# Kernel optimization log

Hardware: AMD Instinct MI355X
Metric: run time of the kernel (lower is better)

## Reference

```python
import jax, jax.numpy as jnp
import numpy as np

SCAD_A = 3.7
PERCENTILE_Q = 0.75
EPS = 1e-8
LAM_HAT = 0.9
PROP_STEP = 4


def setup_inputs() -> dict:
    key = jax.random.key(0)
    ks = jax.random.split(key, 4)
    N, IN, H, OUT = 4096, 512, 256, 64
    p = 32.0 / N  # avg degree ~32 (pre-symmetrization ~64 after OR, still sparse)
    u = jax.random.uniform(ks[0], (N, N))
    Au = u < p
    Asym = Au | Au.T
    eye = jnp.eye(N, dtype=bool)
    A = jnp.where(eye, 0.0, Asym.astype(jnp.float32))  # zero diagonal; add_loops adds I
    X = jax.random.normal(ks[1], (N, IN), dtype=jnp.float32)
    W1 = jax.random.normal(ks[2], (IN, H), dtype=jnp.float32) / np.sqrt(IN)
    b1 = jnp.zeros((H,), dtype=jnp.float32)
    W2 = jax.random.normal(ks[3], (H, OUT), dtype=jnp.float32) / np.sqrt(H)
    b2 = jnp.zeros((OUT,), dtype=jnp.float32)
    log_gamma_0 = jnp.asarray(np.log(3.0), dtype=jnp.float32)
    raw_decay = jnp.asarray(np.log(0.85 / 0.15), dtype=jnp.float32)
    raw_alpha_blend = jnp.asarray(0.0, dtype=jnp.float32)  # sigmoid -> 0.5 blend
    return {"A": A, "X": X, "W1": W1, "b1": b1, "W2": W2, "b2": b2,
            "log_gamma_0": log_gamma_0, "raw_decay": raw_decay,
            "raw_alpha_blend": raw_alpha_blend}


def _scad_weight(y, lam, a):
    # SCAD-derived reweighting: 1 for y<=lam, (a*lam - y)/((a-1)*y) in the middle, 0 beyond a*lam.
    y_safe = jnp.maximum(y, EPS)  # avoid inf/nan in unselected branch (forward value unchanged)
    w_mid = (a * lam - y) / ((a - 1.0) * y_safe)
    return jnp.where(y <= lam, 1.0, jnp.where(y <= a * lam, w_mid, 0.0))


def reference(A, X, W1, b1, W2, b2, log_gamma_0, raw_decay, raw_alpha_blend):
    N = A.shape[0]
    eye = jnp.eye(N, dtype=A.dtype)
    Ahat = A + eye                          # add_loops
    D = Ahat.sum(-1)                        # [N]
    D_sq = jnp.sqrt(D)[:, None]             # [N,1]
    A_tilde = Ahat / (D_sq * D_sq.T)        # sym_norm: D^{-1/2} A D^{-1/2}
    edge_mask = (Ahat > 0) & (eye == 0)     # A_bool & ~I
    has_edges = edge_mask.sum() > 0

    # MLP (eval mode: dropout inactive)
    F0 = jnp.maximum(X @ W1 + b1, 0.0) @ W2 + b2   # [N, out_dim]

    alpha = jax.nn.sigmoid(raw_alpha_blend)
    g0 = jnp.exp(log_gamma_0)
    r = jax.nn.sigmoid(raw_decay)
    lam = 1.0 / LAM_HAT - 1.0

    Fc = F0
    for k in range(PROP_STEP):
        gamma_param_k = g0 * (r ** k)
        Fn = Fc / D_sq
        nrm = jnp.linalg.norm(Fn, axis=-1, keepdims=True)
        Fu = Fn / jnp.maximum(nrm, EPS)     # F.normalize semantics
        y = jnp.clip(1.0 - Fu @ Fu.T, 0.0, 2.0)  # [N,N] cosine distance
        y = jax.lax.stop_gradient(y)        # y.detach()
        y_edges = jnp.where(edge_mask, y, jnp.nan)
        gamma_data_k = jnp.nanquantile(y_edges, PERCENTILE_Q)
        gamma_data_k = jnp.maximum(jnp.where(has_edges, gamma_data_k, 1.0), EPS)
        lam_combined = alpha * (gamma_param_k / SCAD_A) + (1.0 - alpha) * (gamma_data_k / SCAD_A)
        W = _scad_weight(y, lam_combined, SCAD_A)
        W = W * (1.0 - eye)
        W = jnp.where(jnp.isnan(W), 1.0, W)
        Q_hat = ((W * Ahat).sum(-1) / D + lam)[:, None]
        Fc = (W * A_tilde) @ Fc / Q_hat + lam * F0 / Q_hat
    return Fc
```

## Files before the change

### kernel.cpp

```cpp
#include <hip/hip_runtime.h>
#include <math.h>

#define N_NODES 4096
#define IN_DIM  512
#define H_DIM   256
#define OUT_DIM 64
#define SCAD_Af 3.7f
#define EPSf    1e-8f
#define NBINS   8192
#define MAXE    524288
#define MAXD    256
#define KSPLIT  4

__global__ void k_degfill(const float* __restrict__ A, int* __restrict__ tmpcols,
                          int* __restrict__ rowcnt, float* __restrict__ D,
                          float* __restrict__ isD) {
    int i = blockIdx.x;
    __shared__ int cnt;
    if (threadIdx.x == 0) cnt = 0;
    __syncthreads();
    const float* row = A + (size_t)i * N_NODES;
    for (int j = threadIdx.x; j < N_NODES; j += blockDim.x) {
        if (row[j] != 0.0f) {
            int p = atomicAdd(&cnt, 1);
            if (p < MAXD) tmpcols[i * MAXD + p] = j;
        }
    }
    __syncthreads();
    if (threadIdx.x == 0) {
        int t = cnt;
        rowcnt[i] = t;
        float d = (float)t + 1.0f;
        D[i] = d;
        isD[i] = 1.0f / sqrtf(d);
    }
}

__global__ void k_scan(const int* __restrict__ rowcnt, int* __restrict__ rowptr) {
    __shared__ int sh[1024];
    int t = threadIdx.x;
    int v0 = rowcnt[4 * t + 0], v1 = rowcnt[4 * t + 1];
    int v2 = rowcnt[4 * t + 2], v3 = rowcnt[4 * t + 3];
    int s = v0 + v1 + v2 + v3;
    sh[t] = s;
    __syncthreads();
    for (int off = 1; off < 1024; off <<= 1) {
        int x = 0;
        if (t >= off) x = sh[t - off];
        __syncthreads();
        sh[t] += x;
        __syncthreads();
    }
    int excl = sh[t] - s;
    rowptr[4 * t + 0] = excl;
    rowptr[4 * t + 1] = excl + v0;
    rowptr[4 * t + 2] = excl + v0 + v1;
    rowptr[4 * t + 3] = excl + v0 + v1 + v2;
    if (t == 1023) rowptr[N_NODES] = sh[1023];
}

__global__ void k_compact(const int* __restrict__ tmpcols, const int* __restrict__ rowcnt,
                          const int* __restrict__ rowptr, int* __restrict__ colIdx) {
    int i = blockIdx.x;
    int n = rowcnt[i], base = rowptr[i];
    for (int p = threadIdx.x; p < n; p += blockDim.x)
        colIdx[base + p] = tmpcols[i * MAXD + p];
}

__global__ void k_gemm1_part(const float* __restrict__ X, const float* __restrict__ W1,
                             float* __restrict__ part) {
    const int K = IN_DIM, Nn = H_DIM;
    __shared__ float As[16][68];
    __shared__ float Bs[16][64];
    int tx = threadIdx.x & 15, ty = threadIdx.x >> 4;
    int bm = blockIdx.y * 64, bn = blockIdx.x * 64;
    int kbeg = blockIdx.z * (K / KSPLIT), kend = kbeg + K / KSPLIT;
    float acc[4][4] = {};
    for (int k0 = kbeg; k0 < kend; k0 += 16) {
        {
            int r = threadIdx.x >> 2, kv = threadIdx.x & 3;
            float4 v = *(const float4*)(X + (size_t)(bm + r) * K + k0 + kv * 4);
            As[kv * 4 + 0][r] = v.x;
            As[kv * 4 + 1][r] = v.y;
            As[kv * 4 + 2][r] = v.z;
            As[kv * 4 + 3][r] = v.w;
        }
        {
            int kk = threadIdx.x >> 4, nv = threadIdx.x & 15;
            *(float4*)&Bs[kk][nv * 4] =
                *(const float4*)(W1 + (size_t)(k0 + kk) * Nn + bn + nv * 4);
        }
        __syncthreads();
#pragma unroll
        for (int kk = 0; kk < 16; kk++) {
            float a[4], b[4];
#pragma unroll
            for (int u = 0; u < 4; u++) { a[u] = As[kk][ty * 4 + u]; b[u] = Bs[kk][tx * 4 + u]; }
#pragma unroll
            for (int u = 0; u < 4; u++)
#pragma unroll
                for (int v = 0; v < 4; v++) acc[u][v] += a[u] * b[v];
        }
        __syncthreads();
    }
    float* Cm = part + (size_t)blockIdx.z * N_NODES * H_DIM;
#pragma unroll
    for (int u = 0; u < 4; u++) {
        int m = bm + ty * 4 + u;
#pragma unroll
        for (int v = 0; v < 4; v++)
            Cm[(size_t)m * Nn + bn + tx * 4 + v] = acc[u][v];
    }
}

__global__ void k_fuse1(const float* __restrict__ part, const float* __restrict__ bias,
                        float* __restrict__ H1) {
    int idx = blockIdx.x * blockDim.x + threadIdx.x;
    const size_t tot = (size_t)N_NODES * H_DIM / 4;
    const float4* p = (const float4*)part;
    float4 a = p[idx], b = p[tot + idx], c = p[2 * tot + idx], d = p[3 * tot + idx];
    float4 bb = ((const float4*)bias)[idx & (H_DIM / 4 - 1)];
    float4 r;
    r.x = fmaxf(a.x + b.x + c.x + d.x + bb.x, 0.0f);
    r.y = fmaxf(a.y + b.y + c.y + d.y + bb.y, 0.0f);
    r.z = fmaxf(a.z + b.z + c.z + d.z + bb.z, 0.0f);
    r.w = fmaxf(a.w + b.w + c.w + d.w + bb.w, 0.0f);
    ((float4*)H1)[idx] = r;
}

__global__ void k_gemm2(const float* __restrict__ Am, const float* __restrict__ Bm,
                        const float* __restrict__ bias, float* __restrict__ Cm) {
    const int Nn = OUT_DIM, K = H_DIM;
    __shared__ float As[16][68];
    __shared__ float Bs[16][64];
    int tx = threadIdx.x & 15, ty = threadIdx.x >> 4;
    int bm = blockIdx.y * 64, bn = 0;
    float acc[4][4] = {};
    for (int k0 = 0; k0 < K; k0 += 16) {
        {
            int r = threadIdx.x >> 2, kv = threadIdx.x & 3;
            float4 v = *(const float4*)(Am + (size_t)(bm + r) * K + k0 + kv * 4);
            As[kv * 4 + 0][r] = v.x;
            As[kv * 4 + 1][r] = v.y;
            As[kv * 4 + 2][r] = v.z;
            As[kv * 4 + 3][r] = v.w;
        }
        {
            int kk = threadIdx.x >> 4, nv = threadIdx.x & 15;
            *(float4*)&Bs[kk][nv * 4] =
                *(const float4*)(Bm + (size_t)(k0 + kk) * Nn + bn + nv * 4);
        }
        __syncthreads();
#pragma unroll
        for (int kk = 0; kk < 16; kk++) {
            float a[4], b[4];
#pragma unroll
            for (int u = 0; u < 4; u++) { a[u] = As[kk][ty * 4 + u]; b[u] = Bs[kk][tx * 4 + u]; }
#pragma unroll
            for (int u = 0; u < 4; u++)
#pragma unroll
                for (int v = 0; v < 4; v++) acc[u][v] += a[u] * b[v];
        }
        __syncthreads();
    }
#pragma unroll
    for (int u = 0; u < 4; u++) {
        int m = bm + ty * 4 + u;
#pragma unroll
        for (int v = 0; v < 4; v++) {
            int n = bn + tx * 4 + v;
            Cm[(size_t)m * Nn + n] = acc[u][v] + bias[n];
        }
    }
}

__global__ void k_norm(const float* __restrict__ Fc, const float* __restrict__ isD,
                       float* __restrict__ Fu, unsigned int* __restrict__ hist) {
    int gid = blockIdx.x * blockDim.x + threadIdx.x;
    if (gid < NBINS) hist[gid] = 0u;
    int i = gid >> 6, c = gid & 63;
    float fn = Fc[(size_t)i * 64 + c] * isD[i];
    float s = fn * fn;
    for (int off = 32; off; off >>= 1) s += __shfl_xor(s, off, 64);
    float nrm = sqrtf(s);
    Fu[(size_t)i * 64 + c] = fn / fmaxf(nrm, EPSf);
}

__global__ void k_edgehist(const float* __restrict__ Fu, const int* __restrict__ rowptr,
                           const int* __restrict__ colIdx, float* __restrict__ y_e,
                           unsigned int* __restrict__ hist) {
    __shared__ unsigned int hl[NBINS];
    for (int b = threadIdx.x; b < NBINS; b += blockDim.x) hl[b] = 0u;
    __syncthreads();
    int gid = blockIdx.x * blockDim.x + threadIdx.x;
    int i = gid >> 6;
    int lane = threadIdx.x & 63;
    int g = lane >> 2, l = lane & 3;
    int e0 = rowptr[i], e1 = rowptr[i + 1];
    const float4* Fu4 = (const float4*)Fu;
    float4 fi0 = Fu4[i * 16 + l * 4 + 0];
    float4 fi1 = Fu4[i * 16 + l * 4 + 1];
    float4 fi2 = Fu4[i * 16 + l * 4 + 2];
    float4 fi3 = Fu4[i * 16 + l * 4 + 3];
    for (int base = e0; base < e1; base += 16) {
        int e = base + g;
        bool act = e < e1;
        int j = act ? colIdx[e] : i;
        float4 a0 = Fu4[(size_t)j * 16 + l * 4 + 0];
        float4 a1 = Fu4[(size_t)j * 16 + l * 4 + 1];
        float4 a2 = Fu4[(size_t)j * 16 + l * 4 + 2];
        float4 a3 = Fu4[(size_t)j * 16 + l * 4 + 3];
        float s = fi0.x * a0.x + fi0.y * a0.y + fi0.z * a0.z + fi0.w * a0.w
                + fi1.x * a1.x + fi1.y * a1.y + fi1.z * a1.z + fi1.w * a1.w
                + fi2.x * a2.x + fi2.y * a2.y + fi2.z * a2.z + fi2.w * a2.w
                + fi3.x * a3.x + fi3.y * a3.y + fi3.z * a3.z + fi3.w * a3.w;
        s += __shfl_xor(s, 1, 64);
        s += __shfl_xor(s, 2, 64);
        if (act && l == 0) {
            float y = 1.0f - s;
            y = fminf(fmaxf(y, 0.0f), 2.0f);
            y_e[e] = y;
            int bin = (int)(y * (NBINS * 0.5f));
            if (bin > NBINS - 1) bin = NBINS - 1;
            atomicAdd(&hl[bin], 1u);
        }
    }
    __syncthreads();
    for (int b = threadIdx.x; b < NBINS; b += blockDim.x) {
        unsigned int v = hl[b];
        if (v) atomicAdd(&hist[b], v);
    }
}

__device__ __forceinline__ float scad_w(float y, float lamc) {
    if (y <= lamc) return 1.0f;
    if (y <= SCAD_Af * lamc)
        return (SCAD_Af * lamc - y) / ((SCAD_Af - 1.0f) * fmaxf(y, EPSf));
    return 0.0f;
}

__global__ void k_propq(const unsigned int* __restrict__ hist,
                        const int* __restrict__ rowptr, const int* __restrict__ colIdx,
                        const float* __restrict__ y_e, const float* __restrict__ Fc,
                        const float* __restrict__ F0, const float* __restrict__ D,
                        const float* __restrict__ isD,
                        const float* __restrict__ lg0, const float* __restrict__ rdec,
                        const float* __restrict__ ralpha, int kiter,
                        float* __restrict__ Fout) {
    __shared__ unsigned int psum[256];
    __shared__ float vv[2];
    __shared__ float sh_scal;
    int t = threadIdx.x;
    {
        unsigned int cnt[32];
        const uint4* h4 = (const uint4*)hist;
        unsigned int s = 0;
#pragma unroll
        for (int q = 0; q < 8; q++) {
            uint4 v = h4[t * 8 + q];
            cnt[q * 4 + 0] = v.x; cnt[q * 4 + 1] = v.y;
            cnt[q * 4 + 2] = v.z; cnt[q * 4 + 3] = v.w;
            s += v.x + v.y + v.z + v.w;
        }
        psum[t] = s;
        __syncthreads();
        for (int off = 1; off < 256; off <<= 1) {
            unsigned int x = 0;
            if (t >= off) x = psum[t - off];
            __syncthreads();
            psum[t] += x;
            __syncthreads();
        }
        int nE = rowptr[N_NODES];
        double h = 0.75 * (double)(nE - 1);
        long long i0 = (long long)h;
        float frac = (float)(h - (double)i0);
        unsigned int r0 = (unsigned int)i0, r1 = (unsigned int)(i0 + 1);
        unsigned int cum = (t == 0) ? 0u : psum[t - 1];
#pragma unroll
        for (int b = 0; b < 32; b++) {
            unsigned int cn = cnt[b];
            unsigned int lo = cum;
            cum += cn;
            if (cn) {
                float v = ((float)(t * 32 + b) + 0.5f) * (2.0f / (float)NBINS);
                if (lo <= r0 && r0 < cum) vv[0] = v;
                if (lo <= r1 && r1 < cum) vv[1] = v;
            }
        }
        __syncthreads();
        if (t == 0) {
            float gd = vv[0] + frac * (vv[1] - vv[0]);
            gd = fmaxf(gd, EPSf);
            float alpha = 1.0f / (1.0f + expf(-ralpha[0]));
            float g0 = expf(lg0[0]);
            float r = 1.0f / (1.0f + expf(-rdec[0]));
            float gp = g0;
            for (int q = 0; q < kiter; q++) gp *= r;
            sh_scal = alpha * (gp / SCAD_Af) + (1.0f - alpha) * (gd / SCAD_Af);
        }
        __syncthreads();
    }
    float lamc = sh_scal;
    const float lam = (float)(1.0 / 0.9 - 1.0);
    int gid = blockIdx.x * blockDim.x + t;
    int i = gid >> 6, c = gid & 63;
    int e0 = rowptr[i], e1 = rowptr[i + 1];
    float acc = 0.0f, wsum = 0.0f;
    for (int base = e0; base < e1; base += 64) {
        int m = e1 - base; if (m > 64) m = 64;
        int   jl = (c < m) ? colIdx[base + c] : 0;
        float yl = (c < m) ? y_e[base + c] : 9.0f;
        float il = (c < m) ? isD[jl] : 0.0f;
        int tt = 0;
        for (; tt + 4 <= m; tt += 4) {
            int j0 = __shfl(jl, tt, 64),     j1 = __shfl(jl, tt + 1, 64);
            int j2 = __shfl(jl, tt + 2, 64), j3 = __shfl(jl, tt + 3, 64);
            float f0 = Fc[(size_t)j0 * 64 + c], f1 = Fc[(size_t)j1 * 64 + c];
            float f2 = Fc[(size_t)j2 * 64 + c], f3 = Fc[(size_t)j3 * 64 + c];
            float s0 = scad_w(__shfl(yl, tt, 64),     lamc);
            float s1 = scad_w(__shfl(yl, tt + 1, 64), lamc);
            float s2 = scad_w(__shfl(yl, tt + 2, 64), lamc);
            float s3 = scad_w(__shfl(yl, tt + 3, 64), lamc);
            wsum += s0 + s1 + s2 + s3;
            acc += s0 * __shfl(il, tt, 64) * f0 + s1 * __shfl(il, tt + 1, 64) * f1
                 + s2 * __shfl(il, tt + 2, 64) * f2 + s3 * __shfl(il, tt + 3, 64) * f3;
        }
        for (; tt < m; tt++) {
            int   j = __shfl(jl, tt, 64);
            float y = __shfl(yl, tt, 64);
            float w = scad_w(y, lamc);
            wsum += w;
            acc += w * __shfl(il, tt, 64) * Fc[(size_t)j * 64 + c];
        }
    }
    float Q = wsum / D[i] + lam;
    Fout[(size_t)i * 64 + c] = (isD[i] * acc + lam * F0[(size_t)i * 64 + c]) / Q;
}

extern "C" void kernel_launch(void* const* d_in, const int* in_sizes, int n_in,
                              void* d_out, int out_size, void* d_ws, size_t ws_size,
                              hipStream_t stream) {
    const float* A      = (const float*)d_in[0];
    const float* X      = (const float*)d_in[1];
    const float* W1     = (const float*)d_in[2];
    const float* b1     = (const float*)d_in[3];
    const float* W2     = (const float*)d_in[4];
    const float* b2     = (const float*)d_in[5];
    const float* lg0    = (const float*)d_in[6];
    const float* rdec   = (const float*)d_in[7];
    const float* ralpha = (const float*)d_in[8];
    float* out = (float*)d_out;

    char* w = (char*)d_ws;
    size_t off = 0;
    auto carve = [&](size_t bytes) -> char* {
        char* p = w + off;
        off += (bytes + 255) & ~(size_t)255;
        return p;
    };
    int*      rowcnt = (int*)carve(N_NODES * 4);
    int*      rowptr = (int*)carve((N_NODES + 16) * 4);
    int*      colIdx = (int*)carve(MAXE * 4);
    float*    y_e    = (float*)carve(MAXE * 4);
    unsigned* hist   = (unsigned*)carve(NBINS * 4);
    float*    D      = (float*)carve(N_NODES * 4);
    float*    isD    = (float*)carve(N_NODES * 4);
    float*    Fu     = (float*)carve((size_t)N_NODES * 64 * 4);
    float*    H1     = (float*)carve((size_t)N_NODES * H_DIM * 4);
    float*    part   = (float*)carve((size_t)KSPLIT * N_NODES * H_DIM * 4);
    float*    F0     = (float*)carve((size_t)N_NODES * 64 * 4);
    float*    FcA    = (float*)carve((size_t)N_NODES * 64 * 4);
    float*    FcB    = (float*)carve((size_t)N_NODES * 64 * 4);
    int*      tmpcols = (int*)part;

    k_degfill<<<dim3(N_NODES), dim3(256), 0, stream>>>(A, tmpcols, rowcnt, D, isD);
    k_scan<<<dim3(1), dim3(1024), 0, stream>>>(rowcnt, rowptr);
    k_compact<<<dim3(N_NODES), dim3(64), 0, stream>>>(tmpcols, rowcnt, rowptr, colIdx);

    k_gemm1_part<<<dim3(H_DIM / 64, N_NODES / 64, KSPLIT), dim3(256), 0, stream>>>(X, W1, part);
    k_fuse1<<<dim3(N_NODES * H_DIM / 4 / 256), dim3(256), 0, stream>>>(part, b1, H1);
    k_gemm2<<<dim3(1, N_NODES / 64), dim3(256), 0, stream>>>(H1, W2, b2, F0);

    const float* fin = F0;
    float* fouts[4] = {FcA, FcB, FcA, out};
    for (int k = 0; k < 4; k++) {
        k_norm<<<dim3(1024), dim3(256), 0, stream>>>(fin, isD, Fu, hist);
        k_edgehist<<<dim3(1024), dim3(256), 0, stream>>>(Fu, rowptr, colIdx, y_e, hist);
        k_propq<<<dim3(1024), dim3(256), 0, stream>>>(hist, rowptr, colIdx, y_e, fin, F0,
                                                      D, isD, lg0, rdec, ralpha, k, fouts[k]);
        fin = fouts[k];
    }
}
```

Before: 384.3 us.

## Fuse setup kernels, use padded CSR, fold normalization into propagation

Merges the degree scan and GEMM1 into one launch that splits work by block index. It also replaces the prefix-scan/compaction CSR with a fixed-stride padded adjacency (MAXD per row), fuses bias+ReLU+GEMM2 and the first normalization into one kernel, and moves per-iteration normalization into the propagation kernel with double-buffered histograms. This cuts the launch count from 18 to 10 and removes intermediate buffers such as H1. The cost is that GEMM2 now runs as a naive per-thread dot product that re-reads the four partial sums from global memory for every output column. It also drops the MAXD overflow guard on colIdx writes.

```diff
diff --git a/kernel.cpp b/kernel.cpp
--- a/kernel.cpp
+++ b/kernel.cpp
@@ -8,288 +8,241 @@
 #define SCAD_Af 3.7f
 #define EPSf    1e-8f
 #define NBINS   8192
-#define MAXE    524288
 #define MAXD    256
 #define KSPLIT  4
 
-__global__ void k_degfill(const float* __restrict__ A, int* __restrict__ tmpcols,
-                          int* __restrict__ rowcnt, float* __restrict__ D,
-                          float* __restrict__ isD) {
-    int i = blockIdx.x;
-    __shared__ int cnt;
-    if (threadIdx.x == 0) cnt = 0;
-    __syncthreads();
-    const float* row = A + (size_t)i * N_NODES;
-    for (int j = threadIdx.x; j < N_NODES; j += blockDim.x) {
-        if (row[j] != 0.0f) {
-            int p = atomicAdd(&cnt, 1);
-            if (p < MAXD) tmpcols[i * MAXD + p] = j;
-        }
-    }
-    __syncthreads();
-    if (threadIdx.x == 0) {
-        int t = cnt;
-        rowcnt[i] = t;
-        float d = (float)t + 1.0f;
-        D[i] = d;
-        isD[i] = 1.0f / sqrtf(d);
-    }
-}
-
-__global__ void k_scan(const int* __restrict__ rowcnt, int* __restrict__ rowptr) {
-    __shared__ int sh[1024];
-    int t = threadIdx.x;
-    int v0 = rowcnt[4 * t + 0], v1 = rowcnt[4 * t + 1];
-    int v2 = rowcnt[4 * t + 2], v3 = rowcnt[4 * t + 3];
-    int s = v0 + v1 + v2 + v3;
-    sh[t] = s;
-    __syncthreads();
-    for (int off = 1; off < 1024; off <<= 1) {
-        int x = 0;
-        if (t >= off) x = sh[t - off];
-        __syncthreads();
-        sh[t] += x;
-        __syncthreads();
-    }
-    int excl = sh[t] - s;
-    rowptr[4 * t + 0] = excl;
-    rowptr[4 * t + 1] = excl + v0;
-    rowptr[4 * t + 2] = excl + v0 + v1;
-    rowptr[4 * t + 3] = excl + v0 + v1 + v2;
-    if (t == 1023) rowptr[N_NODES] = sh[1023];
-}
-
-__global__ void k_compact(const int* __restrict__ tmpcols, const int* __restrict__ rowcnt,
-                          const int* __restrict__ rowptr, int* __restrict__ colIdx) {
-    int i = blockIdx.x;
-    int n = rowcnt[i], base = rowptr[i];
-    for (int p = threadIdx.x; p < n; p += blockDim.x)
-        colIdx[base + p] = tmpcols[i * MAXD + p];
-}
-
-__global__ void k_gemm1_part(const float* __restrict__ X, const float* __restrict__ W1,
-                             float* __restrict__ part) {
-    const int K = IN_DIM, Nn = H_DIM;
+__device__ __forceinline__ float scad_w(float y, float lamc) {
+    if (y <= lamc) return 1.0f;
+    if (y <= SCAD_Af * lamc)
+        return (SCAD_Af * lamc - y) / ((SCAD_Af - 1.0f) * fmaxf(y, EPSf));
+    return 0.0f;
+}
+
+__global__ __launch_bounds__(256)
+void k_init(const float* __restrict__ A, const float* __restrict__ X,
+            const float* __restrict__ W1, float* __restrict__ part,
+            int* __restrict__ colIdx, int* __restrict__ rowcnt,
+            float* __restrict__ D, float* __restrict__ isD,
+            unsigned int* __restrict__ hist01) {
     __shared__ float As[16][68];
     __shared__ float Bs[16][64];
-    int tx = threadIdx.x & 15, ty = threadIdx.x >> 4;
-    int bm = blockIdx.y * 64, bn = blockIdx.x * 64;
-    int kbeg = blockIdx.z * (K / KSPLIT), kend = kbeg + K / KSPLIT;
-    float acc[4][4] = {};
-    for (int k0 = kbeg; k0 < kend; k0 += 16) {
-        {
-            int r = threadIdx.x >> 2, kv = threadIdx.x & 3;
-            float4 v = *(const float4*)(X + (size_t)(bm + r) * K + k0 + kv * 4);
-            As[kv * 4 + 0][r] = v.x;
-            As[kv * 4 + 1][r] = v.y;
-            As[kv * 4 + 2][r] = v.z;
-            As[kv * 4 + 3][r] = v.w;
-        }
-        {
-            int kk = threadIdx.x >> 4, nv = threadIdx.x & 15;
-            *(float4*)&Bs[kk][nv * 4] =
-                *(const float4*)(W1 + (size_t)(k0 + kk) * Nn + bn + nv * 4);
-        }
-        __syncthreads();
-#pragma unroll
-        for (int kk = 0; kk < 16; kk++) {
-            float a[4], b[4];
-#pragma unroll
-            for (int u = 0; u < 4; u++) { a[u] = As[kk][ty * 4 + u]; b[u] = Bs[kk][tx * 4 + u]; }
-#pragma unroll
-            for (int u = 0; u < 4; u++)
-#pragma unroll
-                for (int v = 0; v < 4; v++) acc[u][v] += a[u] * b[v];
-        }
-        __syncthreads();
-    }
-    float* Cm = part + (size_t)blockIdx.z * N_NODES * H_DIM;
-#pragma unroll
-    for (int u = 0; u < 4; u++) {
-        int m = bm + ty * 4 + u;
-#pragma unroll
-        for (int v = 0; v < 4; v++)
-            Cm[(size_t)m * Nn + bn + tx * 4 + v] = acc[u][v];
-    }
-}
-
-__global__ void k_fuse1(const float* __restrict__ part, const float* __restrict__ bias,
-                        float* __restrict__ H1) {
-    int idx = blockIdx.x * blockDim.x + threadIdx.x;
+    __shared__ int cnt4[4];
+    int tid = threadIdx.x;
+    if (blockIdx.x < 1024) {
+        int blk = blockIdx.x;
+        int bx = blk & 3, by = (blk >> 2) & 63, bz = blk >> 8;
+        int tx = tid & 15, ty = tid >> 4;
+        int bm = by * 64, bn = bx * 64;
+        int kbeg = bz * (IN_DIM / KSPLIT);
+        float acc[4][4] = {};
+        for (int k0 = kbeg; k0 < kbeg + IN_DIM / KSPLIT; k0 += 16) {
+            {
+                int r = tid >> 2, kv = tid & 3;
+                float4 v = *(const float4*)(X + (size_t)(bm + r) * IN_DIM + k0 + kv * 4);
+                As[kv * 4 + 0][r] = v.x;
+                As[kv * 4 + 1][r] = v.y;
+                As[kv * 4 + 2][r] = v.z;
+                As[kv * 4 + 3][r] = v.w;
+            }
+            {
+                int kk = tid >> 4, nv = tid & 15;
+                *(float4*)&Bs[kk][nv * 4] =
+                    *(const float4*)(W1 + (size_t)(k0 + kk) * H_DIM + bn + nv * 4);
+            }
+            __syncthreads();
+#pragma unroll
+            for (int kk = 0; kk < 16; kk++) {
+                float a[4], b[4];
+#pragma unroll
+                for (int u = 0; u < 4; u++) { a[u] = As[kk][ty * 4 + u]; b[u] = Bs[kk][tx * 4 + u]; }
+#pragma unroll
+                for (int u = 0; u < 4; u++)
+#pragma unroll
+                    for (int v = 0; v < 4; v++) acc[u][v] += a[u] * b[v];
+            }
+            __syncthreads();
+        }
+        float* Cm = part + (size_t)bz * N_NODES * H_DIM;
+#pragma unroll
+        for (int u = 0; u < 4; u++) {
+            int m = bm + ty * 4 + u;
+#pragma unroll
+            for (int v = 0; v < 4; v++)
+                Cm[(size_t)m * H_DIM + bn + tx * 4 + v] = acc[u][v];
+        }
+    } else {
+        int bb = blockIdx.x - 1024;
+        int gid2 = bb * 256 + tid;
+        if (gid2 < 2 * NBINS) hist01[gid2] = 0u;
+        int w = tid >> 6, lane = tid & 63;
+        int i = bb * 4 + w;
+        if (lane == 0) cnt4[w] = 0;
+        __syncthreads();
+        const float* row = A + (size_t)i * N_NODES;
+        for (int j = lane; j < N_NODES; j += 64) {
+            if (row[j] != 0.0f) {
+                int p = atomicAdd(&cnt4[w], 1);
+                colIdx[i * MAXD + p] = j;
+            }
+        }
+        __syncthreads();
+        if (lane == 0) {
+            int t = cnt4[w];
+            rowcnt[i] = t;
+            float d = (float)t + 1.0f;
+            D[i] = d;
+            isD[i] = 1.0f / sqrtf(d);
+        }
+    }
+}
+
+__global__ __launch_bounds__(256)
+void k_mlp2(const float* __restrict__ part, const float* __restrict__ b1,
+            const float* __restrict__ W2, const float* __restrict__ b2,
+            const int* __restrict__ rowcnt, const float* __restrict__ isD,
+            float* __restrict__ F0, float* __restrict__ Fu, int* __restrict__ nE) {
+    int tid = threadIdx.x;
+    if (blockIdx.x == 0) {
+        __shared__ unsigned int ps[256];
+        unsigned int s = 0;
+        for (int q = tid; q < N_NODES; q += 256) s += (unsigned int)rowcnt[q];
+        ps[tid] = s;
+        __syncthreads();
+        for (int off = 128; off; off >>= 1) {
+            if (tid < off) ps[tid] += ps[tid + off];
+            __syncthreads();
+        }
+        if (tid == 0) nE[0] = (int)ps[0];
+    }
+    int gid = blockIdx.x * 256 + tid;
+    int i = gid >> 6, c = gid & 63;
     const size_t tot = (size_t)N_NODES * H_DIM / 4;
-    const float4* p = (const float4*)part;
-    float4 a = p[idx], b = p[tot + idx], c = p[2 * tot + idx], d = p[3 * tot + idx];
-    float4 bb = ((const float4*)bias)[idx & (H_DIM / 4 - 1)];
-    float4 r;
-    r.x = fmaxf(a.x + b.x + c.x + d.x + bb.x, 0.0f);
-    r.y = fmaxf(a.y + b.y + c.y + d.y + bb.y, 0.0f);
-    r.z = fmaxf(a.z + b.z + c.z + d.z + bb.z, 0.0f);
-    r.w = fmaxf(a.w + b.w + c.w + d.w + bb.w, 0.0f);
-    ((float4*)H1)[idx] = r;
-}
-
-__global__ void k_gemm2(const float* __restrict__ Am, const float* __restrict__ Bm,
-                        const float* __restrict__ bias, float* __restrict__ Cm) {
-    const int Nn = OUT_DIM, K = H_DIM;
-    __shared__ float As[16][68];
-    __shared__ float Bs[16][64];
-    int tx = threadIdx.x & 15, ty = threadIdx.x >> 4;
-    int bm = blockIdx.y * 64, bn = 0;
-    float acc[4][4] = {};
-    for (int k0 = 0; k0 < K; k0 += 16) {
-        {
-            int r = threadIdx.x >> 2, kv = threadIdx.x & 3;
-            float4 v = *(const float4*)(Am + (size_t)(bm + r) * K + k0 + kv * 4);
-            As[kv * 4 + 0][r] = v.x;
-            As[kv * 4 + 1][r] = v.y;
-            As[kv * 4 + 2][r] = v.z;
-            As[kv * 4 + 3][r] = v.w;
-        }
-        {
-            int kk = threadIdx.x >> 4, nv = threadIdx.x & 15;
-            *(float4*)&Bs[kk][nv * 4] =
-                *(const float4*)(Bm + (size_t)(k0 + kk) * Nn + bn + nv * 4);
-        }
-        __syncthreads();
-#pragma unroll
-        for (int kk = 0; kk < 16; kk++) {
-            float a[4], b[4];
-#pragma unroll
-            for (int u = 0; u < 4; u++) { a[u] = As[kk][ty * 4 + u]; b[u] = Bs[kk][tx * 4 + u]; }
-#pragma unroll
-            for (int u = 0; u < 4; u++)
-#pragma unroll
-                for (int v = 0; v < 4; v++) acc[u][v] += a[u] * b[v];
-        }
-        __syncthreads();
-    }
-#pragma unroll
-    for (int u = 0; u < 4; u++) {
-        int m = bm + ty * 4 + u;
-#pragma unroll
-        for (int v = 0; v < 4; v++) {
-            int n = bn + tx * 4 + v;
-            Cm[(size_t)m * Nn + n] = acc[u][v] + bias[n];
-        }
-    }
-}
-
-__global__ void k_norm(const float* __restrict__ Fc, const float* __restrict__ isD,
-                       float* __restrict__ Fu, unsigned int* __restrict__ hist) {
-    int gid = blockIdx.x * blockDim.x + threadIdx.x;
-    if (gid < NBINS) hist[gid] = 0u;
-    int i = gid >> 6, c = gid & 63;
-    float fn = Fc[(size_t)i * 64 + c] * isD[i];
-    float s = fn * fn;
-    for (int off = 32; off; off >>= 1) s += __shfl_xor(s, off, 64);
-    float nrm = sqrtf(s);
-    Fu[(size_t)i * 64 + c] = fn / fmaxf(nrm, EPSf);
-}
-
-__global__ void k_edgehist(const float* __restrict__ Fu, const int* __restrict__ rowptr,
-                           const int* __restrict__ colIdx, float* __restrict__ y_e,
-                           unsigned int* __restrict__ hist) {
+    const float4* p0 = (const float4*)part + (size_t)i * (H_DIM / 4);
+    const float4* p1 = p0 + tot;
+    const float4* p2 = p1 + tot;
+    const float4* p3 = p2 + tot;
+    const float4* b14 = (const float4*)b1;
+    float a0 = 0, a1 = 0, a2 = 0, a3 = 0;
+    for (int k4 = 0; k4 < H_DIM / 4; k4++) {
+        float4 q0 = p0[k4], q1 = p1[k4], q2 = p2[k4], q3 = p3[k4], bb = b14[k4];
+        float h0 = fmaxf(q0.x + q1.x + q2.x + q3.x + bb.x, 0.0f);
+        float h1 = fmaxf(q0.y + q1.y + q2.y + q3.y + bb.y, 0.0f);
+        float h2 = fmaxf(q0.z + q1.z + q2.z + q3.z + bb.z, 0.0f);
+        float h3 = fmaxf(q0.w + q1.w + q2.w + q3.w + bb.w, 0.0f);
+        a0 += h0 * W2[(k4 * 4 + 0) * OUT_DIM + c];
+        a1 += h1 * W2[(k4 * 4 + 1) * OUT_DIM + c];
+        a2 += h2 * W2[(k4 * 4 + 2) * OUT_DIM + c];
+        a3 += h3 * W2[(k4 * 4 + 3) * OUT_DIM + c];
+    }
+    float f0 = (a0 + a1) + (a2 + a3) + b2[c];
+    F0[(size_t)i * 64 + c] = f0;
+    float fn = f0 * isD[i];
+    float s2 = fn * fn;
+    for (int off = 32; off; off >>= 1) s2 += __shfl_xor(s2, off, 64);
+    Fu[(size_t)i * 64 + c] = fn / fmaxf(sqrtf(s2), EPSf);
+}
+
+__global__ __launch_bounds__(256)
+void k_edgehist(const float* __restrict__ Fu, const int* __restrict__ rowcnt,
+                const int* __restrict__ colIdx, float* __restrict__ y_e,
+                unsigned int* __restrict__ histK) {
     __shared__ unsigned int hl[NBINS];
-    for (int b = threadIdx.x; b < NBINS; b += blockDim.x) hl[b] = 0u;
+    for (int b = threadIdx.x; b < NBINS; b += 256) hl[b] = 0u;
     __syncthreads();
-    int gid = blockIdx.x * blockDim.x + threadIdx.x;
-    int i = gid >> 6;
+    int gid = blockIdx.x * 256 + threadIdx.x;
+    int ri = gid >> 6;
     int lane = threadIdx.x & 63;
-    int g = lane >> 2, l = lane & 3;
-    int e0 = rowptr[i], e1 = rowptr[i + 1];
+    int eg = lane >> 2, el = lane & 3;
+    int deg = rowcnt[ri];
     const float4* Fu4 = (const float4*)Fu;
-    float4 fi0 = Fu4[i * 16 + l * 4 + 0];
-    float4 fi1 = Fu4[i * 16 + l * 4 + 1];
-    float4 fi2 = Fu4[i * 16 + l * 4 + 2];
-    float4 fi3 = Fu4[i * 16 + l * 4 + 3];
-    for (int base = e0; base < e1; base += 16) {
-        int e = base + g;
-        bool act = e < e1;
-        int j = act ? colIdx[e] : i;
-        float4 a0 = Fu4[(size_t)j * 16 + l * 4 + 0];
-        float4 a1 = Fu4[(size_t)j * 16 + l * 4 + 1];
-        float4 a2 = Fu4[(size_t)j * 16 + l * 4 + 2];
-        float4 a3 = Fu4[(size_t)j * 16 + l * 4 + 3];
+    float4 fi0 = Fu4[ri * 16 + el * 4 + 0];
+    float4 fi1 = Fu4[ri * 16 + el * 4 + 1];
+    float4 fi2 = Fu4[ri * 16 + el * 4 + 2];
+    float4 fi3 = Fu4[ri * 16 + el * 4 + 3];
+    for (int base = 0; base < deg; base += 16) {
+        int e = base + eg;
+        bool act = e < deg;
+        int j = act ? colIdx[ri * MAXD + e] : ri;
+        float4 a0 = Fu4[(size_t)j * 16 + el * 4 + 0];
+        float4 a1 = Fu4[(size_t)j * 16 + el * 4 + 1];
+        float4 a2 = Fu4[(size_t)j * 16 + el * 4 + 2];
+        float4 a3 = Fu4[(size_t)j * 16 + el * 4 + 3];
         float s = fi0.x * a0.x + fi0.y * a0.y + fi0.z * a0.z + fi0.w * a0.w
                 + fi1.x * a1.x + fi1.y * a1.y + fi1.z * a1.z + fi1.w * a1.w
                 + fi2.x * a2.x + fi2.y * a2.y + fi2.z * a2.z + fi2.w * a2.w
                 + fi3.x * a3.x + fi3.y * a3.y + fi3.z * a3.z + fi3.w * a3.w;
         s += __shfl_xor(s, 1, 64);
         s += __shfl_xor(s, 2, 64);
-        if (act && l == 0) {
+        if (act && el == 0) {
             float y = 1.0f - s;
             y = fminf(fmaxf(y, 0.0f), 2.0f);
-            y_e[e] = y;
+            y_e[ri * MAXD + e] = y;
             int bin = (int)(y * (NBINS * 0.5f));
             if (bin > NBINS - 1) bin = NBINS - 1;
             atomicAdd(&hl[bin], 1u);
         }
     }
     __syncthreads();
-    for (int b = threadIdx.x; b < NBINS; b += blockDim.x) {
+    for (int b = threadIdx.x; b < NBINS; b += 256) {
         unsigned int v = hl[b];
-        if (v) atomicAdd(&hist[b], v);
-    }
-}
-
-__device__ __forceinline__ float scad_w(float y, float lamc) {
-    if (y <= lamc) return 1.0f;
-    if (y <= SCAD_Af * lamc)
-        return (SCAD_Af * lamc - y) / ((SCAD_Af - 1.0f) * fmaxf(y, EPSf));
-    return 0.0f;
-}
-
-__global__ void k_propq(const unsigned int* __restrict__ hist,
-                        const int* __restrict__ rowptr, const int* __restrict__ colIdx,
-                        const float* __restrict__ y_e, const float* __restrict__ Fc,
-                        const float* __restrict__ F0, const float* __restrict__ D,
-                        const float* __restrict__ isD,
-                        const float* __restrict__ lg0, const float* __restrict__ rdec,
-                        const float* __restrict__ ralpha, int kiter,
-                        float* __restrict__ Fout) {
+        if (v) atomicAdd(&histK[b], v);
+    }
+}
+
+__global__ __launch_bounds__(256)
+void k_propq(const unsigned int* __restrict__ histK, unsigned int* __restrict__ histNext,
+             const int* __restrict__ nEp, const int* __restrict__ rowcnt,
+             const int* __restrict__ colIdx, const float* __restrict__ y_e,
+             const float* __restrict__ Fc, const float* __restrict__ F0,
+             const float* __restrict__ D, const float* __restrict__ isD,
+             const float* __restrict__ lg0, const float* __restrict__ rdec,
+             const float* __restrict__ ralpha, int kiter,
+             float* __restrict__ Fout, float* __restrict__ FuNext) {
     __shared__ unsigned int psum[256];
     __shared__ float vv[2];
     __shared__ float sh_scal;
-    int t = threadIdx.x;
+    int tid = threadIdx.x;
+    int gid = blockIdx.x * 256 + tid;
+    if (gid < NBINS) histNext[gid] = 0u;
     {
         unsigned int cnt[32];
-        const uint4* h4 = (const uint4*)hist;
+        const uint4* h4 = (const uint4*)histK;
         unsigned int s = 0;
 #pragma unroll
         for (int q = 0; q < 8; q++) {
-            uint4 v = h4[t * 8 + q];
+            uint4 v = h4[tid * 8 + q];
             cnt[q * 4 + 0] = v.x; cnt[q * 4 + 1] = v.y;
             cnt[q * 4 + 2] = v.z; cnt[q * 4 + 3] = v.w;
             s += v.x + v.y + v.z + v.w;
         }
-        psum[t] = s;
+        psum[tid] = s;
         __syncthreads();
         for (int off = 1; off < 256; off <<= 1) {
             unsigned int x = 0;
-            if (t >= off) x = psum[t - off];
-            __syncthreads();
-            psum[t] += x;
-            __syncthreads();
-        }
-        int nE = rowptr[N_NODES];
+            if (tid >= off) x = psum[tid - off];
+            __syncthreads();
+            psum[tid] += x;
+            __syncthreads();
+        }
+        int nE = nEp[0];
         double h = 0.75 * (double)(nE - 1);
         long long i0 = (long long)h;
         float frac = (float)(h - (double)i0);
         unsigned int r0 = (unsigned int)i0, r1 = (unsigned int)(i0 + 1);
-        unsigned int cum = (t == 0) ? 0u : psum[t - 1];
+        unsigned int cum = (tid == 0) ? 0u : psum[tid - 1];
 #pragma unroll
         for (int b = 0; b < 32; b++) {
             unsigned int cn = cnt[b];
             unsigned int lo = cum;
             cum += cn;
             if (cn) {
-                float v = ((float)(t * 32 + b) + 0.5f) * (2.0f / (float)NBINS);
+                float v = ((float)(tid * 32 + b) + 0.5f) * (2.0f / (float)NBINS);
                 if (lo <= r0 && r0 < cum) vv[0] = v;
                 if (lo <= r1 && r1 < cum) vv[1] = v;
             }
         }
         __syncthreads();
-        if (t == 0) {
+        if (tid == 0) {
             float gd = vv[0] + frac * (vv[1] - vv[0]);
             gd = fmaxf(gd, EPSf);
             float alpha = 1.0f / (1.0f + expf(-ralpha[0]));
@@ -303,14 +256,13 @@
     }
     float lamc = sh_scal;
     const float lam = (float)(1.0 / 0.9 - 1.0);
-    int gid = blockIdx.x * blockDim.x + t;
     int i = gid >> 6, c = gid & 63;
-    int e0 = rowptr[i], e1 = rowptr[i + 1];
+    int deg = rowcnt[i];
     float acc = 0.0f, wsum = 0.0f;
-    for (int base = e0; base < e1; base += 64) {
-        int m = e1 - base; if (m > 64) m = 64;
-        int   jl = (c < m) ? colIdx[base + c] : 0;
-        float yl = (c < m) ? y_e[base + c] : 9.0f;
+    for (int base = 0; base < deg; base += 64) {
+        int m = deg - base; if (m > 64) m = 64;
+        int   jl = (c < m) ? colIdx[i * MAXD + base + c] : 0;
+        float yl = (c < m) ? y_e[i * MAXD + base + c] : 9.0f;
         float il = (c < m) ? isD[jl] : 0.0f;
         int tt = 0;
         for (; tt + 4 <= m; tt += 4) {
@@ -329,13 +281,18 @@
         for (; tt < m; tt++) {
             int   j = __shfl(jl, tt, 64);
             float y = __shfl(yl, tt, 64);
-            float w = scad_w(y, lamc);
-            wsum += w;
-            acc += w * __shfl(il, tt, 64) * Fc[(size_t)j * 64 + c];
+            float wq = scad_w(y, lamc);
+            wsum += wq;
+            acc += wq * __shfl(il, tt, 64) * Fc[(size_t)j * 64 + c];
         }
     }
     float Q = wsum / D[i] + lam;
-    Fout[(size_t)i * 64 + c] = (isD[i] * acc + lam * F0[(size_t)i * 64 + c]) / Q;
+    float fo = (isD[i] * acc + lam * F0[(size_t)i * 64 + c]) / Q;
+    Fout[(size_t)i * 64 + c] = fo;
+    float fn = fo * isD[i];
+    float s2n = fn * fn;
+    for (int off = 32; off; off >>= 1) s2n += __shfl_xor(s2n, off, 64);
+    FuNext[(size_t)i * 64 + c] = fn / fmaxf(sqrtf(s2n), EPSf);
 }
 
 extern "C" void kernel_launch(void* const* d_in, const int* in_sizes, int n_in,
@@ -350,7 +307,7 @@
     const float* lg0    = (const float*)d_in[6];
     const float* rdec   = (const float*)d_in[7];
     const float* ralpha = (const float*)d_in[8];
-    float* out = (float*)d_out;
+    float* outp = (float*)d_out;
 
     char* w = (char*)d_ws;
     size_t off = 0;
@@ -359,36 +316,31 @@
         off += (bytes + 255) & ~(size_t)255;
         return p;
     };
+    int*      colIdx = (int*)carve((size_t)N_NODES * MAXD * 4);
+    float*    y_e    = (float*)carve((size_t)N_NODES * MAXD * 4);
+    float*    part   = (float*)carve((size_t)KSPLIT * N_NODES * H_DIM * 4);
     int*      rowcnt = (int*)carve(N_NODES * 4);
-    int*      rowptr = (int*)carve((N_NODES + 16) * 4);
-    int*      colIdx = (int*)carve(MAXE * 4);
-    float*    y_e    = (float*)carve(MAXE * 4);
-    unsigned* hist   = (unsigned*)carve(NBINS * 4);
     float*    D      = (float*)carve(N_NODES * 4);
     float*    isD    = (float*)carve(N_NODES * 4);
     float*    Fu     = (float*)carve((size_t)N_NODES * 64 * 4);
-    float*    H1     = (float*)carve((size_t)N_NODES * H_DIM * 4);
-    float*    part   = (float*)carve((size_t)KSPLIT * N_NODES * H_DIM * 4);
     float*    F0     = (float*)carve((size_t)N_NODES * 64 * 4);
     float*    FcA    = (float*)carve((size_t)N_NODES * 64 * 4);
     float*    FcB    = (float*)carve((size_t)N_NODES * 64 * 4);
-    int*      tmpcols = (int*)part;
-
-    k_degfill<<<dim3(N_NODES), dim3(256), 0, stream>>>(A, tmpcols, rowcnt, D, isD);
-    k_scan<<<dim3(1), dim3(1024), 0, stream>>>(rowcnt, rowptr);
-    k_compact<<<dim3(N_NODES), dim3(64), 0, stream>>>(tmpcols, rowcnt, rowptr, colIdx);
-
-    k_gemm1_part<<<dim3(H_DIM / 64, N_NODES / 64, KSPLIT), dim3(256), 0, stream>>>(X, W1, part);
-    k_fuse1<<<dim3(N_NODES * H_DIM / 4 / 256), dim3(256), 0, stream>>>(part, b1, H1);
-    k_gemm2<<<dim3(1, N_NODES / 64), dim3(256), 0, stream>>>(H1, W2, b2, F0);
+    unsigned* hist01 = (unsigned*)carve(2 * NBINS * 4);
+    int*      nE     = (int*)carve(256);
+
+    k_init<<<dim3(2048), dim3(256), 0, stream>>>(A, X, W1, part, colIdx, rowcnt, D, isD, hist01);
+    k_mlp2<<<dim3(1024), dim3(256), 0, stream>>>(part, b1, W2, b2, rowcnt, isD, F0, Fu, nE);
 
     const float* fin = F0;
-    float* fouts[4] = {FcA, FcB, FcA, out};
+    float* fouts[4] = {FcA, FcB, FcA, outp};
     for (int k = 0; k < 4; k++) {
-        k_norm<<<dim3(1024), dim3(256), 0, stream>>>(fin, isD, Fu, hist);
-        k_edgehist<<<dim3(1024), dim3(256), 0, stream>>>(Fu, rowptr, colIdx, y_e, hist);
-        k_propq<<<dim3(1024), dim3(256), 0, stream>>>(hist, rowptr, colIdx, y_e, fin, F0,
-                                                      D, isD, lg0, rdec, ralpha, k, fouts[k]);
+        unsigned* histK    = hist01 + (k & 1) * NBINS;
+        unsigned* histNext = hist01 + ((k + 1) & 1) * NBINS;
+        k_edgehist<<<dim3(1024), dim3(256), 0, stream>>>(Fu, rowcnt, colIdx, y_e, histK);
+        k_propq<<<dim3(1024), dim3(256), 0, stream>>>(histK, histNext, nE, rowcnt, colIdx,
+                                                      y_e, fin, F0, D, isD, lg0, rdec,
+                                                      ralpha, k, fouts[k], Fu);
         fin = fouts[k];
     }
 }
```

Result: no change. 390.3 us (+1.6%).
